# Kernel tuning notes

Hardware: AMD Instinct MI355X
Metric: run time of the kernel (lower is better)

## Reference

```python
import jax, jax.numpy as jnp
import numpy as np

N, E, D, H = 50000, 800000, 128, 8
HD = D // H
EPS = 1e-5


def _layernorm(x, w, b):
    # Custom LayerNorm from the repo: divides by (unbiased std + eps), not sqrt(var+eps)
    mu = x.mean(axis=-1, keepdims=True)
    sd = x.std(axis=-1, keepdims=True, ddof=1)
    return (x - mu) / (sd + EPS) * w + b


def setup_inputs() -> dict:
    key = jax.random.key(0)
    ks = jax.random.split(key, 16)
    s = 1.0 / np.sqrt(D)
    inp = {
        "feats": jax.random.normal(ks[0], (N, D), jnp.float32),
        "edge_index": jax.random.randint(ks[1], (E, 2), 0, N, jnp.int32),
        "Wq": jax.random.normal(ks[2], (D, D), jnp.float32) * s,
        "bq": jnp.zeros((D,), jnp.float32),
        "Wk": jax.random.normal(ks[3], (D, D), jnp.float32) * s,
        "bk": jnp.zeros((D,), jnp.float32),
        "Wv": jax.random.normal(ks[4], (D, D), jnp.float32) * s,
        "bv": jnp.zeros((D,), jnp.float32),
        "Wo": jax.random.normal(ks[5], (D, D), jnp.float32) * s,
        "bo": jnp.zeros((D,), jnp.float32),
        "ln1_w": jnp.ones((D,), jnp.float32),
        "ln1_b": jnp.zeros((D,), jnp.float32),
        "ln2_w": jnp.ones((D,), jnp.float32),
        "ln2_b": jnp.zeros((D,), jnp.float32),
        "W1": jax.random.normal(ks[6], (4 * D, D), jnp.float32) * s,
        "b1": jnp.zeros((4 * D,), jnp.float32),
        "W2": jax.random.normal(ks[7], (D, 4 * D), jnp.float32) * (1.0 / np.sqrt(4 * D)),
        "b2": jnp.zeros((D,), jnp.float32),
    }
    return inp


def reference(feats, edge_index, Wq, bq, Wk, bk, Wv, bv, Wo, bo,
              ln1_w, ln1_b, ln2_w, ln2_b, W1, b1, W2, b2):
    n = feats.shape[0]
    row, col = edge_index[:, 0], edge_index[:, 1]

    # --- multi-head dot-product attention over edges (dropout = identity, eval mode) ---
    x2 = _layernorm(feats, ln1_w, ln1_b)
    q = (x2 @ Wq.T + bq).reshape(n, H, HD)
    k = (x2 @ Wk.T + bk).reshape(n, H, HD)
    v = (x2 @ Wv.T + bv).reshape(n, H, HD)

    # per-edge scores: q[col] . k[row] / sqrt(head_dim)  -> [E, H]
    scores = jnp.einsum('ehd,ehd->eh', q[col], k[row]) / np.sqrt(HD).astype(np.float32)

    # scatter softmax normalized over groups of `row`
    smax = jax.ops.segment_max(scores, row, num_segments=n)       # [N, H]
    ex = jnp.exp(scores - smax[row])                              # [E, H]
    denom = jax.ops.segment_sum(ex, row, num_segments=n)         # [N, H]
    alpha = ex / denom[row]                                       # [E, H]

    # weighted messages, aggregated at col via scatter_add
    msg = alpha[:, :, None] * v[row]                              # [E, H, HD]
    agg = jax.ops.segment_sum(msg, col, num_segments=n).reshape(n, D)
    att = agg @ Wo.T + bo

    feats = feats + att  # residual 1

    # --- MLP block: note ReLU after BOTH linears (fc_dims=[4D, D], D != 1) ---
    x2 = _layernorm(feats, ln2_w, ln2_b)
    h = jax.nn.relu(x2 @ W1.T + b1)
    h = jax.nn.relu(h @ W2.T + b2)
    feats = feats + h  # residual 2
    return feats
```

## Files before the change

kernel.cpp:

```cpp
#include <hip/hip_runtime.h>
#include <hip/hip_bf16.h>
#include <math.h>

#define H_HEADS 8
constexpr float LN_EPS = 1e-5f;
constexpr int NBCH = 64;
constexpr int NSEG = 4;

using short8 = __attribute__((ext_vector_type(8))) short;
using f32x4  = __attribute__((ext_vector_type(4))) float;

__device__ __forceinline__ ushort f2bf(float v){
  __hip_bfloat16 h = __float2bfloat16(v);
  return *reinterpret_cast<ushort*>(&h);
}
__device__ __forceinline__ float bf2f(ushort u){
  return __uint_as_float(((unsigned)u) << 16);
}

__device__ __forceinline__ void stage16(const ushort* g, ushort* l){
  __builtin_amdgcn_global_load_lds((const __attribute__((address_space(1))) unsigned*)g,
                                   (__attribute__((address_space(3))) unsigned*)l,
                                   16, 0, 0);
}

__global__ void ln_kernel(const float* __restrict__ x, const float* __restrict__ w,
                          const float* __restrict__ b, ushort* __restrict__ out, int nrows){
  int wid = threadIdx.x >> 6, lane = threadIdx.x & 63;
  int r = blockIdx.x * (blockDim.x >> 6) + wid;
  if (r >= nrows) return;
  float2 v = ((const float2*)(x + (size_t)r*128))[lane];
  float s = v.x + v.y;
  #pragma unroll
  for (int o = 32; o; o >>= 1) s += __shfl_xor(s, o);
  float mu = s * (1.0f/128.0f);
  float d0 = v.x - mu, d1 = v.y - mu;
  float ss = d0*d0 + d1*d1;
  #pragma unroll
  for (int o = 32; o; o >>= 1) ss += __shfl_xor(ss, o);
  float sd = sqrtf(ss * (1.0f/127.0f));
  float inv = 1.0f / (sd + LN_EPS);
  float2 wv = ((const float2*)w)[lane];
  float2 bv = ((const float2*)b)[lane];
  ushort2 o2 = { f2bf(d0*inv*wv.x + bv.x), f2bf(d1*inv*wv.y + bv.y) };
  ((ushort2*)(out + (size_t)r*128))[lane] = o2;
}

struct CvtArgs { const float* s[6]; ushort* d[6]; int cnt[6]; };
__global__ void cvt6_kernel(CvtArgs a){
  int w = blockIdx.y;
  int i = blockIdx.x*blockDim.x + threadIdx.x;
  if (i < a.cnt[w]) a.d[w][i] = f2bf(a.s[w][i]);
}

template<int K, int RELU, int RESID, int OUT_BF16>
__device__ __forceinline__ void gemm_lds_body(
    const ushort* __restrict__ A, const ushort* __restrict__ W,
    const float* __restrict__ bias, const float* __restrict__ resid,
    void* __restrict__ out, int M, int Nout, int cb, ushort* Wl){
  constexpr int NCH = K / 128;
  int t = threadIdx.x;
  int wid = t >> 6, lane = t & 63;
  int mb = blockIdx.x * 64 + wid * 16;
  int lrow = lane & 15, kgrp = lane >> 4;
  int row = mb + lrow;
  bool rowok = row < M;
  const ushort* arow = A + (size_t)(rowok ? row : (M-1)) * K + kgrp*8;

  f32x4 acc[8] = {};
  short8 af[2][4];

  #pragma unroll
  for (int p = 0; p < 8; ++p){
    int L = p*256 + t;
    int colp = L >> 4, sp = L & 15;
    stage16(W + (size_t)colp*K + ((sp ^ (colp & 7)) << 3),
            (ushort*)((char*)Wl + ((size_t)(p*256 + (t & ~63)))*16));
  }
  #pragma unroll
  for (int kk = 0; kk < 4; ++kk)
    af[0][kk] = *(const short8*)(arow + kk*32);

  #pragma unroll
  for (int ci = 0; ci < NCH; ++ci){
    __syncthreads();
    int cur = ci & 1;
    if (ci + 1 < NCH){
      #pragma unroll
      for (int kk = 0; kk < 4; ++kk)
        af[cur^1][kk] = *(const short8*)(arow + (ci+1)*128 + kk*32);
    }
    #pragma unroll
    for (int kk = 0; kk < 4; ++kk){
      #pragma unroll
      for (int nt = 0; nt < 8; ++nt){
        int colc = nt*16 + lrow;
        int g = kk*4 + kgrp;
        short8 bfv = *(const short8*)((const char*)Wl + colc*256 + ((g ^ (colc & 7))*16));
        acc[nt] = __builtin_amdgcn_mfma_f32_16x16x32_bf16(af[cur][kk], bfv, acc[nt], 0, 0, 0);
      }
    }
    if (ci + 1 < NCH){
      __syncthreads();
      const ushort* Wc = W + (ci+1)*128;
      #pragma unroll
      for (int p = 0; p < 8; ++p){
        int L = p*256 + t;
        int colp = L >> 4, sp = L & 15;
        stage16(Wc + (size_t)colp*K + ((sp ^ (colp & 7)) << 3),
                (ushort*)((char*)Wl + ((size_t)(p*256 + (t & ~63)))*16));
      }
    }
  }

  int r0 = mb + kgrp*4;
  #pragma unroll
  for (int nt = 0; nt < 8; ++nt){
    int c = cb + nt*16 + lrow;
    float bsum = bias[c];
    #pragma unroll
    for (int i = 0; i < 4; ++i){
      int r = r0 + i;
      if (r >= M) continue;
      float v = acc[nt][i] + bsum;
      if (RELU)  v = fmaxf(v, 0.0f);
      if (RESID) v += resid[(size_t)r*Nout + c];
      if (OUT_BF16) ((ushort*)out)[(size_t)r*Nout + c] = f2bf(v);
      else          ((float*)out)[(size_t)r*Nout + c] = v;
    }
  }
}

template<int K, int RELU, int RESID, int OUT_BF16>
__global__ __launch_bounds__(256) void gemm_lds(
    const ushort* __restrict__ A, const ushort* __restrict__ Wfull,
    const float* __restrict__ bias, const float* __restrict__ resid,
    void* __restrict__ out, int M, int Nout){
  __shared__ __align__(16) ushort Wl[16384];
  int cb = blockIdx.y * 128;
  gemm_lds_body<K,RELU,RESID,OUT_BF16>(A, Wfull + (size_t)cb*K, bias, resid, out, M, Nout, cb, Wl);
}

__global__ __launch_bounds__(256) void qkv_lds(
    const ushort* __restrict__ A, const ushort* __restrict__ Wcat,
    const float* __restrict__ bq, const float* __restrict__ bk, const float* __restrict__ bv,
    ushort* __restrict__ qb, ushort* __restrict__ kb, ushort* __restrict__ vb, int M){
  __shared__ __align__(16) ushort Wl[16384];
  int y = blockIdx.y;
  const float* bias = (y==0) ? bq : (y==1) ? bk : bv;
  ushort* out = (y==0) ? qb : (y==1) ? kb : vb;
  gemm_lds_body<128,0,0,1>(A, Wcat + (size_t)y*16384, bias, nullptr, out, M, 128, 0, Wl);
}

__global__ __launch_bounds__(256) void hist_seg2(const int* __restrict__ ei,
    unsigned* __restrict__ copies, int E, int n, int nw, int chunk, int nsb){
  __shared__ unsigned hh[12544];
  int b = blockIdx.x, s = blockIdx.y, t = threadIdx.x;
  int bin0 = s * nsb;
  int bin1 = min(bin0 + nsb, n);
  int words = (bin1 - bin0 + 1) >> 1;
  for (int i = t; i < 2*words; i += 256) hh[i] = 0;
  __syncthreads();
  int lo = b*chunk, hi = min(lo + chunk, E);
  for (int e = lo + t; e < hi; e += 256){
    int2 rc = ((const int2*)ei)[e];
    if (rc.x >= bin0 && rc.x < bin1)
      atomicAdd(&hh[(rc.x - bin0) >> 1], 1u << ((rc.x & 1)*16));
    if (rc.y >= bin0 && rc.y < bin1)
      atomicAdd(&hh[words + ((rc.y - bin0) >> 1)], 1u << ((rc.y & 1)*16));
  }
  __syncthreads();
  unsigned* d0 = copies + (size_t)b*nw + (bin0 >> 1);
  unsigned* d1 = copies + (size_t)(NBCH + b)*nw + (bin0 >> 1);
  for (int i = t; i < words; i += 256){ d0[i] = hh[i]; d1[i] = hh[words + i]; }
}

__global__ __launch_bounds__(256) void scan_fold(const unsigned* __restrict__ copies,
    int* __restrict__ cnt2, int* __restrict__ choff, int n, int nw){
  int y = blockIdx.y;
  int bin = blockIdx.x*256 + threadIdx.x;
  if (bin >= n) return;
  const unsigned* cp = copies + (size_t)y*NBCH*nw + (bin >> 1);
  int sh = (bin & 1)*16;
  int run = 0;
  for (int b = 0; b < NBCH; ++b){
    int c = (int)((cp[(size_t)b*nw] >> sh) & 0xffffu);
    choff[((size_t)y*NBCH + b)*n + bin] = run;
    run += c;
  }
  cnt2[(size_t)y*n + bin] = run;
}

__global__ __launch_bounds__(256) void scan_reduce(const int* __restrict__ cnt0,
                                                   int* __restrict__ partial, int n, int nb){
  const int* cnt = cnt0 + (size_t)blockIdx.y * n;
  int t = threadIdx.x;
  int base = blockIdx.x*1024 + t*4;
  int s = 0;
  #pragma unroll
  for (int j = 0; j < 4; ++j){ int i = base+j; if (i < n) s += cnt[i]; }
  __shared__ int sm[256];
  sm[t] = s; __syncthreads();
  for (int off = 128; off; off >>= 1){
    if (t < off) sm[t] += sm[t+off];
    __syncthreads();
  }
  if (t == 0) partial[blockIdx.y*nb + blockIdx.x] = sm[0];
}

__global__ __launch_bounds__(256) void scan_mid(int* __restrict__ partial, int nb,
                                                int* __restrict__ rptr, int* __restrict__ cptr, int n){
  int y = blockIdx.y;
  int* p = partial + y*nb;
  int t = threadIdx.x;
  __shared__ int sm[256];
  sm[t] = (t < nb) ? p[t] : 0;
  __syncthreads();
  for (int off = 1; off < 256; off <<= 1){
    int v = (t >= off) ? sm[t-off] : 0;
    __syncthreads();
    sm[t] += v;
    __syncthreads();
  }
  if (t < nb) p[t] = (t == 0) ? 0 : sm[t-1];
  if (t == 0) (y ? cptr : rptr)[n] = sm[255];
}

__global__ __launch_bounds__(256) void scan_scatter(const int* __restrict__ cnt0,
                                                    const int* __restrict__ partial,
                                                    int* __restrict__ rptr, int* __restrict__ cptr,
                                                    int n, int nb){
  int y = blockIdx.y;
  const int* cnt = cnt0 + (size_t)y * n;
  int* ptr = y ? cptr : rptr;
  int t = threadIdx.x;
  int base = blockIdx.x*1024 + t*4;
  int v[4]; int s = 0;
  #pragma unroll
  for (int j = 0; j < 4; ++j){ int i = base+j; v[j] = (i<n)?cnt[i]:0; s += v[j]; }
  __shared__ int sm[256];
  sm[t] = s; __syncthreads();
  for (int off = 1; off < 256; off <<= 1){
    int x = (t >= off) ? sm[t-off] : 0;
    __syncthreads();
    sm[t] += x;
    __syncthreads();
  }
  int pre = partial[y*nb + blockIdx.x] + ((t==0)?0:sm[t-1]);
  #pragma unroll
  for (int j = 0; j < 4; ++j){
    int i = base+j;
    if (i < n){ ptr[i] = pre; pre += v[j]; }
  }
}

__global__ __launch_bounds__(256) void fill_r_seg(const int* __restrict__ ei,
    const int* __restrict__ rptr, const int* __restrict__ choffR,
    int* __restrict__ rcol, int* __restrict__ pose, int E, int n, int chunk, int nsb){
  __shared__ unsigned hh[8192];
  int b = blockIdx.x, s = blockIdx.y, t = threadIdx.x;
  int bin0 = s * nsb;
  int bin1 = min(bin0 + nsb, n);
  int words = (bin1 - bin0 + 1) >> 1;
  for (int i = t; i < words; i += 256) hh[i] = 0;
  __syncthreads();
  const int* chb = choffR + (size_t)b*n;
  int lo = b*chunk, hi = min(lo + chunk, E);
  for (int e = lo + t; e < hi; e += 256){
    int2 rc = ((const int2*)ei)[e];
    int bin = rc.x;
    if (bin < bin0 || bin >= bin1) continue;
    int sh = (bin & 1)*16;
    unsigned old = atomicAdd(&hh[(bin - bin0) >> 1], 1u << sh);
    int rank = (int)((old >> sh) & 0xffffu);
    int pos = rptr[bin] + chb[bin] + rank;
    rcol[pos] = rc.y;
    pose[e] = pos;
  }
}

__global__ __launch_bounds__(256) void fill_c_seg(const int* __restrict__ ei,
    const int* __restrict__ cptr, const int* __restrict__ choffC,
    const int* __restrict__ pose, int* __restrict__ crow, int* __restrict__ cposr,
    int E, int n, int chunk, int nsb){
  __shared__ unsigned hh[8192];
  int b = blockIdx.x, s = blockIdx.y, t = threadIdx.x;
  int bin0 = s * nsb;
  int bin1 = min(bin0 + nsb, n);
  int words = (bin1 - bin0 + 1) >> 1;
  for (int i = t; i < words; i += 256) hh[i] = 0;
  __syncthreads();
  const int* chb = choffC + (size_t)b*n;
  int lo = b*chunk, hi = min(lo + chunk, E);
  for (int e = lo + t; e < hi; e += 256){
    int2 rc = ((const int2*)ei)[e];
    int bin = rc.y;
    if (bin < bin0 || bin >= bin1) continue;
    int sh = (bin & 1)*16;
    unsigned old = atomicAdd(&hh[(bin - bin0) >> 1], 1u << sh);
    int rank = (int)((old >> sh) & 0xffffu);
    int pos = cptr[bin] + chb[bin] + rank;
    crow[pos] = rc.x;
    cposr[pose[e]] = pos;
  }
}

__device__ __forceinline__ float qdot16(const ushort* __restrict__ qb, int c, int h,
                                        const float kf[16]){
  const short8* qp = (const short8*)(qb + (size_t)c*128 + h*16);
  short8 q0 = qp[0], q1 = qp[1];
  float s = 0.f;
  #pragma unroll
  for (int i = 0; i < 8; ++i){
    s += bf2f((ushort)q0[i]) * kf[i];
    s += bf2f((ushort)q1[i]) * kf[8+i];
  }
  return s * 0.25f;
}

__global__ void row_softmax_kernel(const ushort* __restrict__ qb, const ushort* __restrict__ kb,
                                   const int* __restrict__ rptr, const int* __restrict__ rcol,
                                   const int* __restrict__ cposr,
                                   ushort* __restrict__ cbuf, int n){
  int wid = threadIdx.x >> 6, lane = threadIdx.x & 63;
  int r = blockIdx.x * (blockDim.x >> 6) + wid;
  if (r >= n) return;
  int lo = rptr[r], hi = rptr[r+1];
  if (lo >= hi) return;
  int h = lane & 7, el = lane >> 3;

  float kf[16];
  {
    const short8* kp = (const short8*)(kb + (size_t)r*128 + h*16);
    short8 k0 = kp[0], k1 = kp[1];
    #pragma unroll
    for (int i = 0; i < 8; ++i){
      kf[i]   = bf2f((ushort)k0[i]);
      kf[8+i] = bf2f((ushort)k1[i]);
    }
  }

  float sreg[8];
  float m = -1e30f;
  #pragma unroll
  for (int ts = 0; ts < 8; ++ts){
    int j = lo + el + ts*8;
    float s = (j < hi) ? qdot16(qb, rcol[j], h, kf) : -1e30f;
    sreg[ts] = s;
    m = fmaxf(m, s);
  }
  for (int j = lo + el + 64; j < hi; j += 8)
    m = fmaxf(m, qdot16(qb, rcol[j], h, kf));
  #pragma unroll
  for (int o = 8; o < 64; o <<= 1) m = fmaxf(m, __shfl_xor(m, o));

  float d = 0.f;
  #pragma unroll
  for (int ts = 0; ts < 8; ++ts){
    int j = lo + el + ts*8;
    if (j < hi){ float e = __expf(sreg[ts] - m); sreg[ts] = e; d += e; }
  }
  for (int j = lo + el + 64; j < hi; j += 8)
    d += __expf(qdot16(qb, rcol[j], h, kf) - m);
  #pragma unroll
  for (int o = 8; o < 64; o <<= 1) d += __shfl_xor(d, o);
  float invd = 1.0f / d;

  #pragma unroll
  for (int ts = 0; ts < 8; ++ts){
    int j = lo + el + ts*8;
    if (j < hi) cbuf[(size_t)cposr[j]*8 + h] = f2bf(sreg[ts] * invd);
  }
  for (int j = lo + el + 64; j < hi; j += 8){
    float s = qdot16(qb, rcol[j], h, kf);
    cbuf[(size_t)cposr[j]*8 + h] = f2bf(__expf(s - m) * invd);
  }
}

__global__ void agg_kernel(const ushort* __restrict__ vb, const ushort* __restrict__ cbuf,
                           const int* __restrict__ cptr, const int* __restrict__ crow,
                           ushort* __restrict__ aggb, int n){
  int wid = threadIdx.x >> 6, lane = threadIdx.x & 63;
  int node = blockIdx.x * (blockDim.x >> 6) + wid;
  if (node >= n) return;
  int lo = cptr[node], hi = cptr[node+1];
  int oct = lane >> 3, l8 = lane & 7;
  float acc[16] = {};
  for (int j = lo + oct; j < hi; j += 8){
    float a = bf2f(cbuf[(size_t)j*8 + l8]);
    int row = crow[j];
    const short8* vp = (const short8*)(vb + (size_t)row*128 + l8*16);
    short8 v0 = vp[0], v1 = vp[1];
    #pragma unroll
    for (int i = 0; i < 8; ++i){
      acc[i]   = fmaf(a, bf2f((ushort)v0[i]), acc[i]);
      acc[8+i] = fmaf(a, bf2f((ushort)v1[i]), acc[8+i]);
    }
  }
  #pragma unroll
  for (int i = 0; i < 16; ++i){
    acc[i] += __shfl_xor(acc[i], 8);
    acc[i] += __shfl_xor(acc[i], 16);
    acc[i] += __shfl_xor(acc[i], 32);
  }
  if (oct == 0){
    short8 o0, o1;
    #pragma unroll
    for (int i = 0; i < 8; ++i){ o0[i] = (short)f2bf(acc[i]); o1[i] = (short)f2bf(acc[8+i]); }
    short8* op = (short8*)(aggb + (size_t)node*128 + l8*16);
    op[0] = o0; op[1] = o1;
  }
}

extern "C" void kernel_launch(void* const* d_in, const int* in_sizes, int n_in,
                              void* d_out, int out_size, void* d_ws, size_t ws_size,
                              hipStream_t stream){
  const float* feats = (const float*)d_in[0];
  const int*   ei    = (const int*)  d_in[1];
  const float* Wq = (const float*)d_in[2];
  const float* bq = (const float*)d_in[3];
  const float* Wk = (const float*)d_in[4];
  const float* bk = (const float*)d_in[5];
  const float* Wv = (const float*)d_in[6];
  const float* bv = (const float*)d_in[7];
  const float* Wo = (const float*)d_in[8];
  const float* bo = (const float*)d_in[9];
  const float* ln1w = (const float*)d_in[10];
  const float* ln1b = (const float*)d_in[11];
  const float* ln2w = (const float*)d_in[12];
  const float* ln2b = (const float*)d_in[13];
  const float* W1 = (const float*)d_in[14];
  const float* b1 = (const float*)d_in[15];
  const float* W2 = (const float*)d_in[16];
  const float* b2 = (const float*)d_in[17];
  float* outp = (float*)d_out;

  int n = in_sizes[0] / 128;
  int E = in_sizes[1] / 2;
  int nw = (n + 1) >> 1;
  int chunk = (E + NBCH - 1) / NBCH;
  int nsb = (((n + NSEG - 1) / NSEG) + 1) & ~1;

  const size_t ND  = (size_t)n * 128;
  const size_t ND2 = ND / 2;
  const size_t EH  = (size_t)E * H_HEADS;

  float* ws = (float*)d_ws;
  ushort* x2b  = (ushort*)ws;
  ushort* qb   = (ushort*)(ws + ND2);
  ushort* kb   = (ushort*)(ws + 2*ND2);
  ushort* vb   = (ushort*)(ws + 3*ND2);
  ushort* cbuf = (ushort*)(ws + 4*ND2);
  ushort* aggb = (ushort*)(ws + 4*ND2 + EH/2);
  int* crow    = (int*)(ws + 5*ND2 + EH/2);
  int* cposr   = crow + E;
  int* rcol    = cposr + E;
  int* pose    = rcol + E;
  int* rptr    = pose + E;
  int* cptr    = rptr + (n + 4);
  int* cnt2    = cptr + (n + 4);
  int* choff   = cnt2 + 2*n;
  unsigned* copies = (unsigned*)(choff + (size_t)2*NBCH*n);
  int* partial = (int*)(copies + (size_t)2*NBCH*nw);
  ushort* wbuf = (ushort*)(partial + 512);
  ushort* Wqb = wbuf;
  ushort* Wkb = Wqb + 16384;
  ushort* Wvb = Wkb + 16384;
  ushort* Wob = Wvb + 16384;
  ushort* W1b = Wob + 16384;
  ushort* W2b = W1b + 65536;
  ushort* h1  = qb;

  CvtArgs ca;
  ca.s[0]=Wq; ca.s[1]=Wk; ca.s[2]=Wv; ca.s[3]=Wo; ca.s[4]=W1; ca.s[5]=W2;
  ca.d[0]=Wqb; ca.d[1]=Wkb; ca.d[2]=Wvb; ca.d[3]=Wob; ca.d[4]=W1b; ca.d[5]=W2b;
  ca.cnt[0]=ca.cnt[1]=ca.cnt[2]=ca.cnt[3]=16384; ca.cnt[4]=ca.cnt[5]=65536;
  cvt6_kernel<<<dim3(65536/256, 6), 256, 0, stream>>>(ca);

  int nb = (n + 1023)/1024;
  hist_seg2 <<<dim3(NBCH,NSEG), 256, 0, stream>>>(ei, copies, E, n, nw, chunk, nsb);
  scan_fold <<<dim3((n+255)/256,2), 256, 0, stream>>>(copies, cnt2, choff, n, nw);
  scan_reduce <<<dim3(nb,2), 256, 0, stream>>>(cnt2, partial, n, nb);
  scan_mid    <<<dim3(1,2),  256, 0, stream>>>(partial, nb, rptr, cptr, n);
  scan_scatter<<<dim3(nb,2), 256, 0, stream>>>(cnt2, partial, rptr, cptr, n, nb);
  fill_r_seg<<<dim3(NBCH,NSEG), 256, 0, stream>>>(ei, rptr, choff,                  rcol, pose, E, n, chunk, nsb);
  fill_c_seg<<<dim3(NBCH,NSEG), 256, 0, stream>>>(ei, cptr, choff + (size_t)NBCH*n, pose, crow, cposr, E, n, chunk, nsb);

  ln_kernel<<<(n+3)/4, 256, 0, stream>>>(feats, ln1w, ln1b, x2b, n);

  int gm = (n + 63)/64;
  qkv_lds<<<dim3(gm,3), 256, 0, stream>>>(x2b, Wqb, bq, bk, bv, qb, kb, vb, n);

  row_softmax_kernel<<<(n+3)/4, 256, 0, stream>>>(qb, kb, rptr, rcol, cposr, cbuf, n);

  agg_kernel<<<(n+3)/4, 256, 0, stream>>>(vb, cbuf, cptr, crow, aggb, n);

  gemm_lds<128,0,1,0><<<dim3(gm,1), 256, 0, stream>>>(aggb, Wob, bo, feats, outp, n, 128);

  ln_kernel<<<(n+3)/4, 256, 0, stream>>>(outp, ln2w, ln2b, x2b, n);

  gemm_lds<128,1,0,1><<<dim3(gm,4), 256, 0, stream>>>(x2b, W1b, b1, nullptr, h1,  n, 512);
  gemm_lds<512,1,1,0><<<dim3(gm,1), 256, 0, stream>>>(h1,  W2b, b2, outp,    outp, n, 128);
}
```

Before: 314.8 us.

## Store Q/K in fp16 with fdot2 scores, narrow chunk offsets, specialise softmax by degree

The QKV GEMM now writes Q and K as fp16 instead of bf16, so the row softmax can compute per-edge scores with packed fp16 dot-product instructions rather than converting bf16 to fp32 and multiplying scalar by scalar. The per-chunk prefix offsets used by the CSR/CSC fill kernels shrink from int32 to uint16, halving that buffer's traffic. The softmax body is templated on a register-tile count chosen from node degree (2, 4 or 8 slots), which cuts wasted predicated work on low-degree rows. The cost is fp16 range and precision risk for Q/K, and uint16 offsets overflow if a node's in-edge or out-edge count exceeds 65535.

```diff
diff --git a/kernel.cpp b/kernel.cpp
--- a/kernel.cpp
+++ b/kernel.cpp
@@ -9,6 +9,16 @@
 
 using short8 = __attribute__((ext_vector_type(8))) short;
 using f32x4  = __attribute__((ext_vector_type(4))) float;
+using half2v = __attribute__((ext_vector_type(2))) _Float16;
+
+#if defined(__has_builtin)
+#  if __has_builtin(__builtin_amdgcn_fdot2)
+#    define HAS_FDOT2 1
+#  endif
+#endif
+#ifndef HAS_FDOT2
+#  define HAS_FDOT2 0
+#endif
 
 __device__ __forceinline__ ushort f2bf(float v){
   __hip_bfloat16 h = __float2bfloat16(v);
@@ -53,7 +63,7 @@
   if (i < a.cnt[w]) a.d[w][i] = f2bf(a.s[w][i]);
 }
 
-template<int K, int RELU, int RESID, int OUT_BF16>
+template<int K, int RELU, int RESID, int OUTMODE>
 __device__ __forceinline__ void gemm_lds_body(
     const ushort* __restrict__ A, const ushort* __restrict__ W,
     const float* __restrict__ bias, const float* __restrict__ resid,
@@ -125,20 +135,23 @@
       float v = acc[nt][i] + bsum;
       if (RELU)  v = fmaxf(v, 0.0f);
       if (RESID) v += resid[(size_t)r*Nout + c];
-      if (OUT_BF16) ((ushort*)out)[(size_t)r*Nout + c] = f2bf(v);
-      else          ((float*)out)[(size_t)r*Nout + c] = v;
+      if (OUTMODE == 1) ((ushort*)out)[(size_t)r*Nout + c] = f2bf(v);
+      else if (OUTMODE == 2){
+        _Float16 hv = (_Float16)v;
+        ((ushort*)out)[(size_t)r*Nout + c] = __builtin_bit_cast(ushort, hv);
+      } else ((float*)out)[(size_t)r*Nout + c] = v;
     }
   }
 }
 
-template<int K, int RELU, int RESID, int OUT_BF16>
+template<int K, int RELU, int RESID, int OUTMODE>
 __global__ __launch_bounds__(256) void gemm_lds(
     const ushort* __restrict__ A, const ushort* __restrict__ Wfull,
     const float* __restrict__ bias, const float* __restrict__ resid,
     void* __restrict__ out, int M, int Nout){
   __shared__ __align__(16) ushort Wl[16384];
   int cb = blockIdx.y * 128;
-  gemm_lds_body<K,RELU,RESID,OUT_BF16>(A, Wfull + (size_t)cb*K, bias, resid, out, M, Nout, cb, Wl);
+  gemm_lds_body<K,RELU,RESID,OUTMODE>(A, Wfull + (size_t)cb*K, bias, resid, out, M, Nout, cb, Wl);
 }
 
 __global__ __launch_bounds__(256) void qkv_lds(
@@ -149,7 +162,10 @@
   int y = blockIdx.y;
   const float* bias = (y==0) ? bq : (y==1) ? bk : bv;
   ushort* out = (y==0) ? qb : (y==1) ? kb : vb;
-  gemm_lds_body<128,0,0,1>(A, Wcat + (size_t)y*16384, bias, nullptr, out, M, 128, 0, Wl);
+  if (y == 2)
+    gemm_lds_body<128,0,0,1>(A, Wcat + (size_t)y*16384, bias, nullptr, out, M, 128, 0, Wl);
+  else
+    gemm_lds_body<128,0,0,2>(A, Wcat + (size_t)y*16384, bias, nullptr, out, M, 128, 0, Wl);
 }
 
 __global__ __launch_bounds__(256) void hist_seg2(const int* __restrict__ ei,
@@ -176,7 +192,7 @@
 }
 
 __global__ __launch_bounds__(256) void scan_fold(const unsigned* __restrict__ copies,
-    int* __restrict__ cnt2, int* __restrict__ choff, int n, int nw){
+    int* __restrict__ cnt2, ushort* __restrict__ choff, int n, int nw){
   int y = blockIdx.y;
   int bin = blockIdx.x*256 + threadIdx.x;
   if (bin >= n) return;
@@ -185,7 +201,7 @@
   int run = 0;
   for (int b = 0; b < NBCH; ++b){
     int c = (int)((cp[(size_t)b*nw] >> sh) & 0xffffu);
-    choff[((size_t)y*NBCH + b)*n + bin] = run;
+    choff[((size_t)y*NBCH + b)*n + bin] = (ushort)run;
     run += c;
   }
   cnt2[(size_t)y*n + bin] = run;
@@ -255,7 +271,7 @@
 }
 
 __global__ __launch_bounds__(256) void fill_r_seg(const int* __restrict__ ei,
-    const int* __restrict__ rptr, const int* __restrict__ choffR,
+    const int* __restrict__ rptr, const ushort* __restrict__ choffR,
     int* __restrict__ rcol, int* __restrict__ pose, int E, int n, int chunk, int nsb){
   __shared__ unsigned hh[8192];
   int b = blockIdx.x, s = blockIdx.y, t = threadIdx.x;
@@ -264,7 +280,7 @@
   int words = (bin1 - bin0 + 1) >> 1;
   for (int i = t; i < words; i += 256) hh[i] = 0;
   __syncthreads();
-  const int* chb = choffR + (size_t)b*n;
+  const ushort* chb = choffR + (size_t)b*n;
   int lo = b*chunk, hi = min(lo + chunk, E);
   for (int e = lo + t; e < hi; e += 256){
     int2 rc = ((const int2*)ei)[e];
@@ -273,14 +289,14 @@
     int sh = (bin & 1)*16;
     unsigned old = atomicAdd(&hh[(bin - bin0) >> 1], 1u << sh);
     int rank = (int)((old >> sh) & 0xffffu);
-    int pos = rptr[bin] + chb[bin] + rank;
+    int pos = rptr[bin] + (int)chb[bin] + rank;
     rcol[pos] = rc.y;
     pose[e] = pos;
   }
 }
 
 __global__ __launch_bounds__(256) void fill_c_seg(const int* __restrict__ ei,
-    const int* __restrict__ cptr, const int* __restrict__ choffC,
+    const int* __restrict__ cptr, const ushort* __restrict__ choffC,
     const int* __restrict__ pose, int* __restrict__ crow, int* __restrict__ cposr,
     int E, int n, int chunk, int nsb){
   __shared__ unsigned hh[8192];
@@ -290,7 +306,7 @@
   int words = (bin1 - bin0 + 1) >> 1;
   for (int i = t; i < words; i += 256) hh[i] = 0;
   __syncthreads();
-  const int* chb = choffC + (size_t)b*n;
+  const ushort* chb = choffC + (size_t)b*n;
   int lo = b*chunk, hi = min(lo + chunk, E);
   for (int e = lo + t; e < hi; e += 256){
     int2 rc = ((const int2*)ei)[e];
@@ -299,23 +315,74 @@
     int sh = (bin & 1)*16;
     unsigned old = atomicAdd(&hh[(bin - bin0) >> 1], 1u << sh);
     int rank = (int)((old >> sh) & 0xffffu);
-    int pos = cptr[bin] + chb[bin] + rank;
+    int pos = cptr[bin] + (int)chb[bin] + rank;
     crow[pos] = rc.x;
     cposr[pose[e]] = pos;
   }
 }
 
-__device__ __forceinline__ float qdot16(const ushort* __restrict__ qb, int c, int h,
-                                        const float kf[16]){
-  const short8* qp = (const short8*)(qb + (size_t)c*128 + h*16);
-  short8 q0 = qp[0], q1 = qp[1];
+__device__ __forceinline__ float qdot16h(const ushort* __restrict__ qb, int c, int h,
+                                         const half2v* kf2){
+  const int4* qp = (const int4*)(qb + (size_t)c*128 + h*16);
+  int4 a = qp[0], b = qp[1];
+  int qa[8] = {a.x, a.y, a.z, a.w, b.x, b.y, b.z, b.w};
   float s = 0.f;
+#if HAS_FDOT2
+  #pragma unroll
+  for (int i = 0; i < 8; ++i)
+    s = __builtin_amdgcn_fdot2(__builtin_bit_cast(half2v, qa[i]), kf2[i], s, false);
+#else
   #pragma unroll
   for (int i = 0; i < 8; ++i){
-    s += bf2f((ushort)q0[i]) * kf[i];
-    s += bf2f((ushort)q1[i]) * kf[8+i];
-  }
+    half2v q2 = __builtin_bit_cast(half2v, qa[i]);
+    s += (float)q2.x * (float)kf2[i].x + (float)q2.y * (float)kf2[i].y;
+  }
+#endif
   return s * 0.25f;
+}
+
+template<int NS>
+__device__ __forceinline__ void softmax_rows(const ushort* __restrict__ qb,
+    const int* __restrict__ rcol, const int* __restrict__ cposr,
+    ushort* __restrict__ cbuf, const half2v* kf2, int lo, int hi, int h, int el){
+  float sreg[NS];
+  float m = -1e30f;
+  #pragma unroll
+  for (int ts = 0; ts < NS; ++ts){
+    int j = lo + el + ts*8;
+    float s = (j < hi) ? qdot16h(qb, rcol[j], h, kf2) : -1e30f;
+    sreg[ts] = s;
+    m = fmaxf(m, s);
+  }
+  if (NS == 8)
+    for (int j = lo + el + 64; j < hi; j += 8)
+      m = fmaxf(m, qdot16h(qb, rcol[j], h, kf2));
+  #pragma unroll
+  for (int o = 8; o < 64; o <<= 1) m = fmaxf(m, __shfl_xor(m, o));
+
+  float d = 0.f;
+  #pragma unroll
+  for (int ts = 0; ts < NS; ++ts){
+    int j = lo + el + ts*8;
+    if (j < hi){ float e = __expf(sreg[ts] - m); sreg[ts] = e; d += e; }
+  }
+  if (NS == 8)
+    for (int j = lo + el + 64; j < hi; j += 8)
+      d += __expf(qdot16h(qb, rcol[j], h, kf2) - m);
+  #pragma unroll
+  for (int o = 8; o < 64; o <<= 1) d += __shfl_xor(d, o);
+  float invd = 1.0f / d;
+
+  #pragma unroll
+  for (int ts = 0; ts < NS; ++ts){
+    int j = lo + el + ts*8;
+    if (j < hi) cbuf[(size_t)cposr[j]*8 + h] = f2bf(sreg[ts] * invd);
+  }
+  if (NS == 8)
+    for (int j = lo + el + 64; j < hi; j += 8){
+      float s = qdot16h(qb, rcol[j], h, kf2);
+      cbuf[(size_t)cposr[j]*8 + h] = f2bf(__expf(s - m) * invd);
+    }
 }
 
 __global__ void row_softmax_kernel(const ushort* __restrict__ qb, const ushort* __restrict__ kb,
@@ -329,52 +396,24 @@
   if (lo >= hi) return;
   int h = lane & 7, el = lane >> 3;
 
-  float kf[16];
+  half2v kf2[8];
   {
-    const short8* kp = (const short8*)(kb + (size_t)r*128 + h*16);
-    short8 k0 = kp[0], k1 = kp[1];
-    #pragma unroll
-    for (int i = 0; i < 8; ++i){
-      kf[i]   = bf2f((ushort)k0[i]);
-      kf[8+i] = bf2f((ushort)k1[i]);
-    }
-  }
-
-  float sreg[8];
-  float m = -1e30f;
-  #pragma unroll
-  for (int ts = 0; ts < 8; ++ts){
-    int j = lo + el + ts*8;
-    float s = (j < hi) ? qdot16(qb, rcol[j], h, kf) : -1e30f;
-    sreg[ts] = s;
-    m = fmaxf(m, s);
-  }
-  for (int j = lo + el + 64; j < hi; j += 8)
-    m = fmaxf(m, qdot16(qb, rcol[j], h, kf));
-  #pragma unroll
-  for (int o = 8; o < 64; o <<= 1) m = fmaxf(m, __shfl_xor(m, o));
-
-  float d = 0.f;
-  #pragma unroll
-  for (int ts = 0; ts < 8; ++ts){
-    int j = lo + el + ts*8;
-    if (j < hi){ float e = __expf(sreg[ts] - m); sreg[ts] = e; d += e; }
-  }
-  for (int j = lo + el + 64; j < hi; j += 8)
-    d += __expf(qdot16(qb, rcol[j], h, kf) - m);
-  #pragma unroll
-  for (int o = 8; o < 64; o <<= 1) d += __shfl_xor(d, o);
-  float invd = 1.0f / d;
-
-  #pragma unroll
-  for (int ts = 0; ts < 8; ++ts){
-    int j = lo + el + ts*8;
-    if (j < hi) cbuf[(size_t)cposr[j]*8 + h] = f2bf(sreg[ts] * invd);
-  }
-  for (int j = lo + el + 64; j < hi; j += 8){
-    float s = qdot16(qb, rcol[j], h, kf);
-    cbuf[(size_t)cposr[j]*8 + h] = f2bf(__expf(s - m) * invd);
-  }
+    const int4* kp = (const int4*)(kb + (size_t)r*128 + h*16);
+    int4 k0 = kp[0], k1 = kp[1];
+    kf2[0] = __builtin_bit_cast(half2v, k0.x);
+    kf2[1] = __builtin_bit_cast(half2v, k0.y);
+    kf2[2] = __builtin_bit_cast(half2v, k0.z);
+    kf2[3] = __builtin_bit_cast(half2v, k0.w);
+    kf2[4] = __builtin_bit_cast(half2v, k1.x);
+    kf2[5] = __builtin_bit_cast(half2v, k1.y);
+    kf2[6] = __builtin_bit_cast(half2v, k1.z);
+    kf2[7] = __builtin_bit_cast(half2v, k1.w);
+  }
+
+  int deg = hi - lo;
+  if (deg <= 16)      softmax_rows<2>(qb, rcol, cposr, cbuf, kf2, lo, hi, h, el);
+  else if (deg <= 32) softmax_rows<4>(qb, rcol, cposr, cbuf, kf2, lo, hi, h, el);
+  else                softmax_rows<8>(qb, rcol, cposr, cbuf, kf2, lo, hi, h, el);
 }
 
 __global__ void agg_kernel(const ushort* __restrict__ vb, const ushort* __restrict__ cbuf,
@@ -459,7 +498,7 @@
   int* rptr    = pose + E;
   int* cptr    = rptr + (n + 4);
   int* cnt2    = cptr + (n + 4);
-  int* choff   = cnt2 + 2*n;
+  ushort* choff = (ushort*)(cnt2 + 2*n);
   unsigned* copies = (unsigned*)(choff + (size_t)2*NBCH*n);
   int* partial = (int*)(copies + (size_t)2*NBCH*nw);
   ushort* wbuf = (ushort*)(partial + 512);
```

Result: faster. 305.2 us (-3.0%).
